# Kernel optimization log

Measured on AMD Instinct MI355X. Metric: run time of the kernel, lower is better.

Reference implementation:

```python
import jax, jax.numpy as jnp
import numpy as np

DIM_MODEL = 512
DIM_HEAD = 64


def setup_inputs() -> dict:
    key = jax.random.key(0)
    ks = jax.random.split(key, 7)
    B, S = 4, 4096
    x = jax.random.normal(ks[0], (B, S, DIM_MODEL), dtype=jnp.float32)
    mask = jnp.ones((B, 1, S), dtype=jnp.int32)
    # torch Linear init: U(-1/sqrt(fan_in), 1/sqrt(fan_in)); stored as (in, out) for x @ W
    bound = 1.0 / np.sqrt(DIM_MODEL)
    Wq = jax.random.uniform(ks[1], (DIM_MODEL, DIM_HEAD), minval=-bound, maxval=bound, dtype=jnp.float32)
    bq = jax.random.uniform(ks[2], (DIM_HEAD,), minval=-bound, maxval=bound, dtype=jnp.float32)
    Wk = jax.random.uniform(ks[3], (DIM_MODEL, DIM_HEAD), minval=-bound, maxval=bound, dtype=jnp.float32)
    bk = jax.random.uniform(ks[4], (DIM_HEAD,), minval=-bound, maxval=bound, dtype=jnp.float32)
    Wv = jax.random.uniform(ks[5], (DIM_MODEL, DIM_HEAD), minval=-bound, maxval=bound, dtype=jnp.float32)
    bv = jax.random.uniform(ks[6], (DIM_HEAD,), minval=-bound, maxval=bound, dtype=jnp.float32)
    return {"x": x, "mask": mask, "Wq": Wq, "bq": bq, "Wk": Wk, "bk": bk, "Wv": Wv, "bv": bv}


def reference(x, mask, Wq, bq, Wk, bk, Wv, bv):
    # single-head QKV projection
    q = x @ Wq + bq  # (B, S, Dh)
    k = x @ Wk + bk
    v = x @ Wv + bv
    dot_scale = jnp.sqrt(jnp.float32(DIM_HEAD))
    # explicit O(S^2) score matrix, softmax over keys
    scores = jnp.einsum("bqd,bkd->bqk", q, k) / dot_scale  # (B, S, S)
    attn = jax.nn.softmax(scores, axis=-1)
    # faithful to source: mask applied AFTER softmax with -inf fill
    attn = jnp.where(mask == 0, jnp.float32(-jnp.inf), attn)
    return jnp.einsum("bqk,bkd->bqd", attn, v)  # (B, S, Dh)
```

## Files before the change

### kernel.cpp

```cpp
#include <hip/hip_runtime.h>
#include <hip/hip_bf16.h>

typedef _Float16 half8v __attribute__((ext_vector_type(8)));
typedef _Float16 half4v __attribute__((ext_vector_type(4)));
typedef _Float16 half2v __attribute__((ext_vector_type(2)));
typedef __fp16   fp16x2 __attribute__((ext_vector_type(2)));
typedef __attribute__((ext_vector_type(4))) float floatx4;

#define LOG2E_OVER_8 0.18033688011112042f


__device__ __forceinline__ void gload_lds16(const void* g, void* l) {
    __builtin_amdgcn_global_load_lds(
        (const __attribute__((address_space(1))) void*)(unsigned long long)g,
        (__attribute__((address_space(3))) void*)(unsigned)(unsigned long long)l,
        16, 0, 0);
}

__global__ __launch_bounds__(256) void wtrans_k(const float* __restrict__ Wq,
                                                const float* __restrict__ Wk,
                                                const float* __restrict__ Wv,
                                                _Float16* __restrict__ Wt) {
    int idx = blockIdx.x * 256 + threadIdx.x;
    int p = idx >> 15, rem = idx & 32767;
    int k = rem >> 6;
    int n = rem & 63;
    const float* W = (p == 0) ? Wq : ((p == 1) ? Wk : Wv);
    int ctg = p * 4 + (n >> 4), m = n & 15;
    int kc = k >> 5, quad = (k >> 3) & 3, j = k & 7;
    Wt[(((ctg << 4) + kc) * 64 + (quad << 4) + m) * 8 + j] = (_Float16)W[k * 64 + n];
}

#define XS_STRIDE 536
__global__ __launch_bounds__(256) void proj_k(const float* __restrict__ x,
                                              const _Float16* __restrict__ Wt,
                                              const float* __restrict__ bq,
                                              const float* __restrict__ bk,
                                              const float* __restrict__ bv,
                                              _Float16* __restrict__ Qh,
                                              _Float16* __restrict__ Kh,
                                              _Float16* __restrict__ Vh) {
    __shared__ _Float16 xs[2][16 * XS_STRIDE];

    int tid = threadIdx.x, l = tid & 63, wv = tid >> 6;
    int m = l & 15, quad = l >> 4;
    int row0 = blockIdx.x * 32;

#pragma unroll
    for (int s = 0; s < 2; s++)
#pragma unroll
        for (int i = 0; i < 8; i++) {
            int idx = tid + i * 256;
            int row = idx >> 7, c4 = idx & 127;
            float4 v = *(const float4*)(x + (row0 + s * 16 + row) * 512 + c4 * 4);
            union { half2v h[2]; uint2 u; } cv;
            cv.h[0][0] = (_Float16)v.x; cv.h[0][1] = (_Float16)v.y;
            cv.h[1][0] = (_Float16)v.z; cv.h[1][1] = (_Float16)v.w;
            *(uint2*)(xs[s] + row * XS_STRIDE + c4 * 4) = cv.u;
        }
    __syncthreads();

    const _Float16* arow0 = xs[0] + m * XS_STRIDE + quad * 8;
    const _Float16* arow1 = xs[1] + m * XS_STRIDE + quad * 8;

    floatx4 acc[2][3];
#pragma unroll
    for (int s = 0; s < 2; s++)
#pragma unroll
        for (int i = 0; i < 3; i++) acc[s][i] = (floatx4)(0.f);

#pragma unroll 4
    for (int kc = 0; kc < 16; kc++) {
        half8v a0 = *(const half8v*)(arow0 + kc * 32);
        half8v a1 = *(const half8v*)(arow1 + kc * 32);
#pragma unroll
        for (int ct = 0; ct < 3; ct++) {
            int ctg = wv * 3 + ct;
            half8v b = *(const half8v*)(Wt + (((ctg << 4) + kc) * 64 + l) * 8);
            acc[0][ct] = __builtin_amdgcn_mfma_f32_16x16x32_f16(a0, b, acc[0][ct], 0, 0, 0);
            acc[1][ct] = __builtin_amdgcn_mfma_f32_16x16x32_f16(a1, b, acc[1][ct], 0, 0, 0);
        }
    }

#pragma unroll
    for (int s = 0; s < 2; s++) {
        int rowb = row0 + s * 16;
#pragma unroll
        for (int ct = 0; ct < 3; ct++) {
            int ctg = wv * 3 + ct;
            int col = ctg * 16 + m;
            float bias = (ctg < 4) ? bq[col] : ((ctg < 8) ? bk[col - 64] : bv[col - 128]);
            if (ctg < 8) {
                _Float16* dst = (ctg < 4) ? Qh : Kh;
                float scl = (ctg < 4) ? LOG2E_OVER_8 : 1.0f;
                int dd = (ctg & 3) * 16 + m;
                int c = dd >> 5, quadQ = (dd >> 3) & 3, j = dd & 7;
#pragma unroll
                for (int r = 0; r < 4; r++) {
                    int row = rowb + quad * 4 + r;
                    int chunk = ((row >> 4) << 1) + c;
                    dst[(chunk * 64 + quadQ * 16 + (row & 15)) * 8 + j] =
                        (_Float16)((acc[s][ct][r] + bias) * scl);
                }
            } else {
                int dt = ctg - 8;
                int t64 = rowb >> 6, ktp = (rowb >> 5) & 1, half = (rowb >> 4) & 1;
                int chunk = t64 * 8 + dt * 2 + ktp;
                union { _Float16 h[4]; unsigned long long u; } pk;
#pragma unroll
                for (int r = 0; r < 4; r++) pk.h[r] = (_Float16)(acc[s][ct][r] + bias);
                *(unsigned long long*)(Vh + (chunk * 64 + quad * 16 + m) * 8 + half * 4) = pk.u;
            }
        }
    }
}

template <int NT>
__global__ __launch_bounds__(256) void attn_k(const _Float16* __restrict__ Qh,
                                              const _Float16* __restrict__ Kh,
                                              const _Float16* __restrict__ Vh,
                                              const int* __restrict__ mask,
                                              _Float16* __restrict__ Np,
                                              float* __restrict__ Dp,
                                              int gshift) {
    __shared__ __align__(16) uint4 stage_lds[2][1024];

    int tid = threadIdx.x, l = tid & 63, wv = tid >> 6;
    int m = l & 15, quad = l >> 4;
    int bid = blockIdx.x;
    int grp = bid & ((1 << gshift) - 1), qblk = bid >> gshift;
    int os = grp >> 2, b = grp & 3;
    int q0 = qblk * 128 + wv * 32;

    const int* maskb = mask + b * 4096 + os * (NT * 64);
    int az = 0;
#pragma unroll
    for (int i = 0; i < NT; i++) az |= (maskb[l + i * 64] == 0);
    const bool hasz = __any(az);

    int qt_g = (b * 4096 + q0) >> 4;
    half8v qf[2][2];
#pragma unroll
    for (int qt = 0; qt < 2; qt++)
#pragma unroll
        for (int c = 0; c < 2; c++)
            qf[qt][c] = *(const half8v*)(Qh + (((qt_g + qt) * 2 + c) * 64 + l) * 8);

    int tb0 = (b * 64 + os * NT) * 512;
    const uint4* kh4 = (const uint4*)Kh + tb0;
    const uint4* vh4 = (const uint4*)Vh + tb0;

    floatx4 oacc[2][4];
#pragma unroll
    for (int qt = 0; qt < 2; qt++)
#pragma unroll
        for (int dt = 0; dt < 4; dt++) oacc[qt][dt] = (floatx4)(0.f);
    float dl[2] = {0.f, 0.f};

#pragma unroll
    for (int i = 0; i < 2; i++) {
        int idx = wv * 128 + i * 64 + l;
        gload_lds16(kh4 + idx, &stage_lds[0][0] + idx);
        gload_lds16(vh4 + idx, &stage_lds[0][512] + idx);
    }
    __syncthreads();

#pragma unroll 2
    for (int t = 0; t < NT; t++) {
        int cur = t & 1;
        if (t + 1 < NT) {
            const uint4* ksrc = kh4 + (t + 1) * 512;
            const uint4* vsrc = vh4 + (t + 1) * 512;
            uint4* kb = &stage_lds[cur ^ 1][0];
            uint4* vb = &stage_lds[cur ^ 1][512];
#pragma unroll
            for (int i = 0; i < 2; i++) {
                int idx = wv * 128 + i * 64 + l;
                gload_lds16(ksrc + idx, kb + idx);
                gload_lds16(vsrc + idx, vb + idx);
            }
        }
        const uint4* kt4 = &stage_lds[cur][0];
        const uint4* vt4 = &stage_lds[cur][512];
        uint4 vv[4];
#pragma unroll
        for (int sub = 0; sub < 4; sub++) {
            union { uint4 u; half8v h; } ku0, ku1;
            ku0.u = kt4[(sub * 2 + 0) * 64 + l];
            ku1.u = kt4[(sub * 2 + 1) * 64 + l];
            if ((sub & 1) == 0) {
#pragma unroll
                for (int dt = 0; dt < 4; dt++)
                    vv[dt] = vt4[(dt * 2 + (sub >> 1)) * 64 + l];
            }
            half4v pb[2];
#pragma unroll
            for (int qt = 0; qt < 2; qt++) {
                floatx4 sf = (floatx4)(0.f);
                sf = __builtin_amdgcn_mfma_f32_16x16x32_f16(ku0.h, qf[qt][0], sf, 0, 0, 0);
                sf = __builtin_amdgcn_mfma_f32_16x16x32_f16(ku1.h, qf[qt][1], sf, 0, 0, 0);
                float p0 = exp2f(sf[0]), p1 = exp2f(sf[1]);
                float p2 = exp2f(sf[2]), p3 = exp2f(sf[3]);
                dl[qt] += (p0 + p1) + (p2 + p3);
                if (hasz) {
                    int kg = t * 64 + sub * 16 + quad * 4;
                    if (maskb[kg + 0] == 0) p0 = -__builtin_inff();
                    if (maskb[kg + 1] == 0) p1 = -__builtin_inff();
                    if (maskb[kg + 2] == 0) p2 = -__builtin_inff();
                    if (maskb[kg + 3] == 0) p3 = -__builtin_inff();
                }
                union { fp16x2 h[2]; half4v h4; } pu;
                pu.h[0] = __builtin_amdgcn_cvt_pkrtz(p0, p1);
                pu.h[1] = __builtin_amdgcn_cvt_pkrtz(p2, p3);
                pb[qt] = pu.h4;
            }
#pragma unroll
            for (int dt = 0; dt < 4; dt++) {
                union { uint4 u; half4v h[2]; } vc; vc.u = vv[dt];
                half4v va = vc.h[sub & 1];
                oacc[0][dt] = __builtin_amdgcn_mfma_f32_16x16x16f16(va, pb[0], oacc[0][dt], 0, 0, 0);
                oacc[1][dt] = __builtin_amdgcn_mfma_f32_16x16x16f16(va, pb[1], oacc[1][dt], 0, 0, 0);
            }
        }
        __syncthreads();
    }

    float* Tw = (float*)&stage_lds[0][0] + wv * (16 * 68);
    int rowb = os * 16384 + b * 4096 + q0;
#pragma unroll
    for (int qt = 0; qt < 2; qt++) {
        float dqt = dl[qt];
        dqt += __shfl_xor(dqt, 16, 64);
        dqt += __shfl_xor(dqt, 32, 64);
        if (l < 16) Dp[rowb + qt * 16 + l] = dqt;
#pragma unroll
        for (int dt = 0; dt < 4; dt++)
#pragma unroll
            for (int r = 0; r < 4; r++)
                Tw[m * 68 + dt * 16 + quad * 4 + r] = oacc[qt][dt][r];
        __builtin_amdgcn_s_waitcnt(0);
#pragma unroll
        for (int g = 0; g < 4; g++) {
            int idx = g * 64 + l;
            int row = idx >> 4, c4 = (idx & 15) * 4;
            float4 v = *(const float4*)(Tw + row * 68 + c4);
            union { half4v h; unsigned long long u; } pk;
            pk.h[0] = (_Float16)v.x; pk.h[1] = (_Float16)v.y;
            pk.h[2] = (_Float16)v.z; pk.h[3] = (_Float16)v.w;
            *(unsigned long long*)(Np + (size_t)(rowb + qt * 16 + row) * 64 + c4) = pk.u;
        }
        __builtin_amdgcn_s_waitcnt(0);
    }
}

__global__ __launch_bounds__(256) void combine_k(const _Float16* __restrict__ Np,
                                                 const float* __restrict__ Dp,
                                                 float* __restrict__ out,
                                                 int spl) {
    int g4 = blockIdx.x * 256 + threadIdx.x;
    int row = g4 >> 4;
    float4 nu = make_float4(0.f, 0.f, 0.f, 0.f);
    float d = 0.f;
    for (int sp = 0; sp < spl; sp++) {
        union { unsigned long long u; half4v h; } v;
        v.u = *(const unsigned long long*)(Np + ((size_t)sp << 20) + (size_t)g4 * 4);
        nu.x += (float)v.h[0]; nu.y += (float)v.h[1];
        nu.z += (float)v.h[2]; nu.w += (float)v.h[3];
        d += Dp[sp * 16384 + row];
    }
    float inv = 1.0f / d;
    ((float4*)out)[g4] = make_float4(nu.x * inv, nu.y * inv, nu.z * inv, nu.w * inv);
}

extern "C" void kernel_launch(void* const* d_in, const int* in_sizes, int n_in,
                              void* d_out, int out_size, void* d_ws, size_t ws_size,
                              hipStream_t stream) {
    const float* x  = (const float*)d_in[0];
    const int* mask = (const int*)d_in[1];
    const float* Wq = (const float*)d_in[2];
    const float* bq = (const float*)d_in[3];
    const float* Wk = (const float*)d_in[4];
    const float* bk = (const float*)d_in[5];
    const float* Wv = (const float*)d_in[6];
    const float* bv = (const float*)d_in[7];
    float* out = (float*)d_out;

    char* ws = (char*)d_ws;
    _Float16* Wt = (_Float16*)(ws);
    _Float16* Qh = (_Float16*)(ws + 0x40000);
    _Float16* Kh = (_Float16*)(ws + 0x240000);
    _Float16* Vh = (_Float16*)(ws + 0x440000);
    float*    Dp = (float*)(ws + 0x640000);
    _Float16* Np = (_Float16*)(ws + 0x740000);

    wtrans_k<<<384, 256, 0, stream>>>(Wq, Wk, Wv, Wt);
    proj_k<<<512, 256, 0, stream>>>(x, Wt, bq, bk, bv, Qh, Kh, Vh);
    attn_k<8><<<32 * 32, 256, 0, stream>>>(Qh, Kh, Vh, mask, Np, Dp, 5);
    combine_k<<<1024, 256, 0, stream>>>(Np, Dp, out, 8);
}
```

Before: 137.2 us.

## Use 16x16x32 MFMA for PV and compute softmax denominator with MFMA

The inner key loop now handles 32 keys per step instead of 16. The P·V product uses the wider 16x16x32 f16 MFMA, so it needs half as many matrix instructions. The per-lane VALU sum of exponentials and the final cross-lane shuffles are replaced by an MFMA against a vector of ones, which accumulates the row denominators on the matrix unit. In exchange, the denominator is now summed from fp16-rounded probabilities after the mask fill, so it changes numerically and semantically when the mask contains zeros. Holding more K and V fragments at once also raises register pressure.

Result: faster. 133.5 us (-2.7%).

```diff
diff --git a/kernel.cpp b/kernel.cpp
--- a/kernel.cpp
+++ b/kernel.cpp
@@ -146,6 +146,10 @@
         for (int c = 0; c < 2; c++)
             qf[qt][c] = *(const half8v*)(Qh + (((qt_g + qt) * 2 + c) * 64 + l) * 8);
 
+    half8v ones8;
+#pragma unroll
+    for (int i = 0; i < 8; i++) ones8[i] = (_Float16)1.0f;
+
     int tb0 = (b * 64 + os * NT) * 512;
     const uint4* kh4 = (const uint4*)Kh + tb0;
     const uint4* vh4 = (const uint4*)Vh + tb0;
@@ -155,7 +159,7 @@
     for (int qt = 0; qt < 2; qt++)
 #pragma unroll
         for (int dt = 0; dt < 4; dt++) oacc[qt][dt] = (floatx4)(0.f);
-    float dl[2] = {0.f, 0.f};
+    floatx4 oden[2] = {(floatx4)(0.f), (floatx4)(0.f)};
 
 #pragma unroll
     for (int i = 0; i < 2; i++) {
@@ -182,44 +186,45 @@
         }
         const uint4* kt4 = &stage_lds[cur][0];
         const uint4* vt4 = &stage_lds[cur][512];
-        uint4 vv[4];
-#pragma unroll
-        for (int sub = 0; sub < 4; sub++) {
-            union { uint4 u; half8v h; } ku0, ku1;
-            ku0.u = kt4[(sub * 2 + 0) * 64 + l];
-            ku1.u = kt4[(sub * 2 + 1) * 64 + l];
-            if ((sub & 1) == 0) {
-#pragma unroll
-                for (int dt = 0; dt < 4; dt++)
-                    vv[dt] = vt4[(dt * 2 + (sub >> 1)) * 64 + l];
+#pragma unroll
+        for (int sp = 0; sp < 2; sp++) {
+            union { uint4 u; half8v h; } kk[4];
+#pragma unroll
+            for (int i = 0; i < 4; i++)
+                kk[i].u = kt4[(sp * 4 + i) * 64 + l];
+            uint4 vv[4];
+#pragma unroll
+            for (int dt = 0; dt < 4; dt++)
+                vv[dt] = vt4[(dt * 2 + sp) * 64 + l];
+            half8v pb8[2];
+#pragma unroll
+            for (int qt = 0; qt < 2; qt++) {
+                union { fp16x2 h2[4]; half8v h8; } pu;
+#pragma unroll
+                for (int se = 0; se < 2; se++) {
+                    floatx4 sf = (floatx4)(0.f);
+                    sf = __builtin_amdgcn_mfma_f32_16x16x32_f16(kk[se * 2 + 0].h, qf[qt][0], sf, 0, 0, 0);
+                    sf = __builtin_amdgcn_mfma_f32_16x16x32_f16(kk[se * 2 + 1].h, qf[qt][1], sf, 0, 0, 0);
+                    float p0 = exp2f(sf[0]), p1 = exp2f(sf[1]);
+                    float p2 = exp2f(sf[2]), p3 = exp2f(sf[3]);
+                    if (hasz) {
+                        int kg = t * 64 + (sp * 2 + se) * 16 + quad * 4;
+                        if (maskb[kg + 0] == 0) p0 = -__builtin_inff();
+                        if (maskb[kg + 1] == 0) p1 = -__builtin_inff();
+                        if (maskb[kg + 2] == 0) p2 = -__builtin_inff();
+                        if (maskb[kg + 3] == 0) p3 = -__builtin_inff();
+                    }
+                    pu.h2[se * 2 + 0] = __builtin_amdgcn_cvt_pkrtz(p0, p1);
+                    pu.h2[se * 2 + 1] = __builtin_amdgcn_cvt_pkrtz(p2, p3);
+                }
+                pb8[qt] = pu.h8;
+                oden[qt] = __builtin_amdgcn_mfma_f32_16x16x32_f16(ones8, pb8[qt], oden[qt], 0, 0, 0);
             }
-            half4v pb[2];
-#pragma unroll
-            for (int qt = 0; qt < 2; qt++) {
-                floatx4 sf = (floatx4)(0.f);
-                sf = __builtin_amdgcn_mfma_f32_16x16x32_f16(ku0.h, qf[qt][0], sf, 0, 0, 0);
-                sf = __builtin_amdgcn_mfma_f32_16x16x32_f16(ku1.h, qf[qt][1], sf, 0, 0, 0);
-                float p0 = exp2f(sf[0]), p1 = exp2f(sf[1]);
-                float p2 = exp2f(sf[2]), p3 = exp2f(sf[3]);
-                dl[qt] += (p0 + p1) + (p2 + p3);
-                if (hasz) {
-                    int kg = t * 64 + sub * 16 + quad * 4;
-                    if (maskb[kg + 0] == 0) p0 = -__builtin_inff();
-                    if (maskb[kg + 1] == 0) p1 = -__builtin_inff();
-                    if (maskb[kg + 2] == 0) p2 = -__builtin_inff();
-                    if (maskb[kg + 3] == 0) p3 = -__builtin_inff();
-                }
-                union { fp16x2 h[2]; half4v h4; } pu;
-                pu.h[0] = __builtin_amdgcn_cvt_pkrtz(p0, p1);
-                pu.h[1] = __builtin_amdgcn_cvt_pkrtz(p2, p3);
-                pb[qt] = pu.h4;
-            }
 #pragma unroll
             for (int dt = 0; dt < 4; dt++) {
-                union { uint4 u; half4v h[2]; } vc; vc.u = vv[dt];
-                half4v va = vc.h[sub & 1];
-                oacc[0][dt] = __builtin_amdgcn_mfma_f32_16x16x16f16(va, pb[0], oacc[0][dt], 0, 0, 0);
-                oacc[1][dt] = __builtin_amdgcn_mfma_f32_16x16x16f16(va, pb[1], oacc[1][dt], 0, 0, 0);
+                union { uint4 u; half8v h; } vc; vc.u = vv[dt];
+                oacc[0][dt] = __builtin_amdgcn_mfma_f32_16x16x32_f16(vc.h, pb8[0], oacc[0][dt], 0, 0, 0);
+                oacc[1][dt] = __builtin_amdgcn_mfma_f32_16x16x32_f16(vc.h, pb8[1], oacc[1][dt], 0, 0, 0);
             }
         }
         __syncthreads();
@@ -229,10 +234,7 @@
     int rowb = os * 16384 + b * 4096 + q0;
 #pragma unroll
     for (int qt = 0; qt < 2; qt++) {
-        float dqt = dl[qt];
-        dqt += __shfl_xor(dqt, 16, 64);
-        dqt += __shfl_xor(dqt, 32, 64);
-        if (l < 16) Dp[rowb + qt * 16 + l] = dqt;
+        if (l < 16) Dp[rowb + qt * 16 + l] = oden[qt][0];
 #pragma unroll
         for (int dt = 0; dt < 4; dt++)
 #pragma unroll
```
